# Optimization experiments

Measured on AMD Instinct MI355X. Metric: run time of the kernel, lower is better.

## Reference

```python
import jax, jax.numpy as jnp
import numpy as np

B, N, D, H, C = 4, 512, 128, 128, 3


def setup_inputs() -> dict:
    key = jax.random.key(0)
    k1, k2, k3, k4, k5 = jax.random.split(key, 5)
    s1 = 1.0 / np.sqrt(2 * D)  # torch Linear default init scale (uniform bound); randn is fine for a numerics baseline
    s2 = 1.0 / np.sqrt(H)
    return {
        "h_dense": jax.random.normal(k1, (B, N, D), dtype=jnp.float32),
        "W1": jax.random.normal(k2, (H, 2 * D), dtype=jnp.float32) * s1,
        "b1": jax.random.normal(k3, (H,), dtype=jnp.float32) * s1,
        "W2": jax.random.normal(k4, (C, H), dtype=jnp.float32) * s2,
        "b2": jax.random.normal(k5, (C,), dtype=jnp.float32) * s2,
    }


def reference(h_dense, W1, b1, W2, b2):
    # Linear(concat(h_src, h_dst)) == h_src @ W1[:, :D].T + h_dst @ W1[:, D:].T + b1
    # which avoids materializing the (B, N, N, 2D) concat tensor (same math).
    d = h_dense.shape[-1]
    a = jnp.einsum("bnd,hd->bnh", h_dense, W1[:, :d])  # src projection (B, N, H)
    b = jnp.einsum("bnd,hd->bnh", h_dense, W1[:, d:])  # dst projection (B, N, H)
    pre = a[:, :, None, :] + b[:, None, :, :] + b1      # (B, N, N, H)
    act = jax.nn.silu(pre)
    logits = jnp.einsum("bijh,ch->bijc", act, W2) + b2  # (B, N, N, C)
    # symmetrize over the pair axes (dropout is identity in eval mode)
    return (logits + jnp.swapaxes(logits, 1, 2)) * 0.5
```

## Files before the change

### kernel.cpp

```cpp
#include <hip/hip_runtime.h>
#include <hip/hip_fp16.h>

#define B_ 4
#define N_ 512
#define D_ 128
#define H_ 128
#define C_ 3

#define NEG_LOG2E   (-1.4426950408889634f)
#define NEG_HALF_LN2 (-0.34657359027997264f)

typedef _Float16 half8  __attribute__((ext_vector_type(8)));
typedef _Float16 half4v __attribute__((ext_vector_type(4)));

__device__ __forceinline__ float exp2_fast(float x) {
    return __builtin_amdgcn_exp2f(x);
}

__global__ __launch_bounds__(256) void proj_gemm(
    const float* __restrict__ hd, const float* __restrict__ W1,
    const float* __restrict__ b1, _Float16* __restrict__ At, _Float16* __restrict__ Bt)
{
    __shared__ float hsT[64][36];
    __shared__ float wt [64][68];
    const int m0      = blockIdx.x * 32;
    const int by      = blockIdx.y;
    const int halfSel = by >> 1;
    const int wrow0   = (by & 1) * 64;

    const int t  = threadIdx.x;
    const int r  = t >> 4, c4 = t & 15;
    const int tx = t & 15, ty = t >> 4;

    float acc[2][4] = {};

    for (int kc = 0; kc < 2; ++kc) {
        if (kc) __syncthreads();
        #pragma unroll
        for (int i = 0; i < 2; ++i) {
            const int m = r + 16 * i;
            float4 v = *(const float4*)&hd[(m0 + m) * D_ + kc * 64 + 4 * c4];
            hsT[4 * c4 + 0][m] = v.x; hsT[4 * c4 + 1][m] = v.y;
            hsT[4 * c4 + 2][m] = v.z; hsT[4 * c4 + 3][m] = v.w;
        }
        #pragma unroll
        for (int i = 0; i < 4; ++i) {
            const int o = r + 16 * i;
            float4 v = *(const float4*)&W1[(wrow0 + o) * (2 * D_) + halfSel * D_ + kc * 64 + 4 * c4];
            wt[4 * c4 + 0][o] = v.x; wt[4 * c4 + 1][o] = v.y;
            wt[4 * c4 + 2][o] = v.z; wt[4 * c4 + 3][o] = v.w;
        }
        __syncthreads();
        #pragma unroll 8
        for (int k = 0; k < 64; ++k) {
            float2 a  = *(const float2*)&hsT[k][2 * ty];
            float4 bv = *(const float4*)&wt [k][4 * tx];
            acc[0][0] = fmaf(a.x, bv.x, acc[0][0]); acc[0][1] = fmaf(a.x, bv.y, acc[0][1]);
            acc[0][2] = fmaf(a.x, bv.z, acc[0][2]); acc[0][3] = fmaf(a.x, bv.w, acc[0][3]);
            acc[1][0] = fmaf(a.y, bv.x, acc[1][0]); acc[1][1] = fmaf(a.y, bv.y, acc[1][1]);
            acc[1][2] = fmaf(a.y, bv.z, acc[1][2]); acc[1][3] = fmaf(a.y, bv.w, acc[1][3]);
        }
    }

    _Float16* dst = halfSel ? Bt : At;
    const int ocol = wrow0 + 4 * tx;
    float4 bias = make_float4(0.f, 0.f, 0.f, 0.f);
    if (!halfSel) bias = *(const float4*)&b1[ocol];
    #pragma unroll
    for (int i = 0; i < 2; ++i) {
        half4v o;
        o[0] = (_Float16)((acc[i][0] + bias.x) * NEG_LOG2E);
        o[1] = (_Float16)((acc[i][1] + bias.y) * NEG_LOG2E);
        o[2] = (_Float16)((acc[i][2] + bias.z) * NEG_LOG2E);
        o[3] = (_Float16)((acc[i][3] + bias.w) * NEG_LOG2E);
        *(half4v*)&dst[(m0 + 2 * ty + i) * H_ + ocol] = o;
    }
}

__global__ __launch_bounds__(256, 4) void pair_kernel(
    const _Float16* __restrict__ At, const _Float16* __restrict__ Bt,
    const float* __restrict__ W2, const float* __restrict__ b2,
    float* __restrict__ out)
{
    __shared__ _Float16 tiles[8][16 * 64];
    const int T = N_ / 16;
    int tp = blockIdx.x;
    const int b = blockIdx.y;
    int I = 0;
    while (tp >= T - I) { tp -= T - I; ++I; }
    const int J = I + tp;

    const int tid = threadIdx.x;
    const int stile = tid >> 6;
    const int srow  = (tid >> 2) & 15;
    const int scc   = tid & 3;
    const _Float16* gsrc = ((stile & 2) ? Bt : At)
        + (size_t)(b * N_ + ((stile & 1) ? J : I) * 16 + srow) * H_;
    _Float16* ybase = &tiles[stile][srow * 64];
    _Float16* ebase = &tiles[stile + 4][srow * 64];
    const int sxor = srow & 7;

    const int ti = tid >> 4, tj = tid & 15;
    const int xI = ti & 7, xJ = tj & 7;

    float acc0a = 0.f, acc1a = 0.f, acc2a = 0.f;
    float acc0b = 0.f, acc1b = 0.f, acc2b = 0.f;

    for (int ph = 0; ph < 2; ++ph) {
        if (ph) __syncthreads();
        #pragma unroll
        for (int q = 0; q < 2; ++q) {
            const int c = scc + 4 * q;
            half8 yv = *(const half8*)&gsrc[ph * 64 + c * 8];
            half8 ev;
            #pragma unroll
            for (int e = 0; e < 8; ++e)
                ev[e] = (_Float16)exp2_fast((float)yv[e]);
            const int cs = (c ^ sxor) * 8;
            *(half8*)&ybase[cs] = yv;
            *(half8*)&ebase[cs] = ev;
        }
        __syncthreads();

        #pragma unroll 2
        for (int c = 0; c < 8; ++c) {
            const int oI = ti * 64 + ((c ^ xI) * 8);
            const int oJ = tj * 64 + ((c ^ xJ) * 8);
            half8 yAI = *(const half8*)&tiles[0][oI];
            half8 yAJ = *(const half8*)&tiles[1][oJ];
            half8 yBI = *(const half8*)&tiles[2][oI];
            half8 yBJ = *(const half8*)&tiles[3][oJ];
            half8 eAI = *(const half8*)&tiles[4][oI];
            half8 eAJ = *(const half8*)&tiles[5][oJ];
            half8 eBI = *(const half8*)&tiles[6][oI];
            half8 eBJ = *(const half8*)&tiles[7][oJ];

            half8 y1 = yAI + yBJ;
            half8 y2 = yAJ + yBI;
            half8 e1 = eAI * eBJ;
            half8 e2 = eAJ * eBI;
            half8 d1 = e1 + (_Float16)1.0f;
            half8 d2 = e2 + (_Float16)1.0f;
            half8 pp = d1 * d2;
            half8 num = y1 * d2 + y2 * d1;

            const int hb = ph * 64 + c * 8;
            float4 w0a = *(const float4*)&W2[hb],          w0b = *(const float4*)&W2[hb + 4];
            float4 w1a = *(const float4*)&W2[H_ + hb],     w1b = *(const float4*)&W2[H_ + hb + 4];
            float4 w2a = *(const float4*)&W2[2 * H_ + hb], w2b = *(const float4*)&W2[2 * H_ + hb + 4];
            const float w0[8] = {w0a.x, w0a.y, w0a.z, w0a.w, w0b.x, w0b.y, w0b.z, w0b.w};
            const float w1[8] = {w1a.x, w1a.y, w1a.z, w1a.w, w1b.x, w1b.y, w1b.z, w1b.w};
            const float w2[8] = {w2a.x, w2a.y, w2a.z, w2a.w, w2b.x, w2b.y, w2b.z, w2b.w};

            #pragma unroll
            for (int e = 0; e < 8; e += 2) {
                const float sa = (float)num[e]     * __builtin_amdgcn_rcpf((float)pp[e]);
                const float sb = (float)num[e + 1] * __builtin_amdgcn_rcpf((float)pp[e + 1]);
                acc0a = fmaf(sa, w0[e],     acc0a);
                acc1a = fmaf(sa, w1[e],     acc1a);
                acc2a = fmaf(sa, w2[e],     acc2a);
                acc0b = fmaf(sb, w0[e + 1], acc0b);
                acc1b = fmaf(sb, w1[e + 1], acc1b);
                acc2b = fmaf(sb, w2[e + 1], acc2b);
            }
        }
    }

    const float o0 = fmaf(NEG_HALF_LN2, acc0a + acc0b, b2[0]);
    const float o1 = fmaf(NEG_HALF_LN2, acc1a + acc1b, b2[1]);
    const float o2 = fmaf(NEG_HALF_LN2, acc2a + acc2b, b2[2]);
    const int i = I * 16 + ti, j = J * 16 + tj;
    float* p1 = out + ((size_t)(b * N_ + i) * N_ + j) * C_;
    float* p2 = out + ((size_t)(b * N_ + j) * N_ + i) * C_;
    p1[0] = o0; p1[1] = o1; p1[2] = o2;
    p2[0] = o0; p2[1] = o1; p2[2] = o2;
}

extern "C" void kernel_launch(void* const* d_in, const int* in_sizes, int n_in,
                              void* d_out, int out_size, void* d_ws, size_t ws_size,
                              hipStream_t stream) {
    const float* hd = (const float*)d_in[0];
    const float* W1 = (const float*)d_in[1];
    const float* b1 = (const float*)d_in[2];
    const float* W2 = (const float*)d_in[3];
    const float* b2 = (const float*)d_in[4];
    float* out = (float*)d_out;

    _Float16* At = (_Float16*)d_ws;
    _Float16* Bt = At + B_ * N_ * H_;

    proj_gemm<<<dim3((B_ * N_) / 32, 4), dim3(256), 0, stream>>>(hd, W1, b1, At, Bt);

    const int T = N_ / 16;
    pair_kernel<<<dim3(T * (T + 1) / 2, B_), dim3(256), 0, stream>>>(At, Bt, W2, b2, out);
}
```

Baseline: 39.25 us.

## Enlarge pair tiles to 32x32 with 2x2 register blocking per thread

Each pair_kernel block now covers a 32x32 (i,j) tile, and each thread computes four output pairs. Every LDS-loaded row vector is reused across two pairs, and the W2 loads and exp2 preprocessing are amortized over more outputs. The cost is four times fewer blocks (528 vs 2112 over B=4), occupancy lowered to 2 waves, more registers and 32 KB of LDS per block. Diagonal blocks still do redundant symmetric work.

```diff
diff --git a/kernel.cpp b/kernel.cpp
--- a/kernel.cpp
+++ b/kernel.cpp
@@ -77,13 +77,13 @@
     }
 }
 
-__global__ __launch_bounds__(256, 4) void pair_kernel(
+__global__ __launch_bounds__(256, 2) void pair_kernel(
     const _Float16* __restrict__ At, const _Float16* __restrict__ Bt,
     const float* __restrict__ W2, const float* __restrict__ b2,
     float* __restrict__ out)
 {
-    __shared__ _Float16 tiles[8][16 * 64];
-    const int T = N_ / 16;
+    __shared__ _Float16 tiles[8][32 * 64];
+    const int T = N_ / 32;
     int tp = blockIdx.x;
     const int b = blockIdx.y;
     int I = 0;
@@ -92,10 +92,11 @@
 
     const int tid = threadIdx.x;
     const int stile = tid >> 6;
-    const int srow  = (tid >> 2) & 15;
-    const int scc   = tid & 3;
+    const int lane  = tid & 63;
+    const int srow  = lane >> 1;
+    const int shalf = lane & 1;
     const _Float16* gsrc = ((stile & 2) ? Bt : At)
-        + (size_t)(b * N_ + ((stile & 1) ? J : I) * 16 + srow) * H_;
+        + (size_t)(b * N_ + ((stile & 1) ? J : I) * 32 + srow) * H_;
     _Float16* ybase = &tiles[stile][srow * 64];
     _Float16* ebase = &tiles[stile + 4][srow * 64];
     const int sxor = srow & 7;
@@ -103,14 +104,13 @@
     const int ti = tid >> 4, tj = tid & 15;
     const int xI = ti & 7, xJ = tj & 7;
 
-    float acc0a = 0.f, acc1a = 0.f, acc2a = 0.f;
-    float acc0b = 0.f, acc1b = 0.f, acc2b = 0.f;
+    float acc[4][3] = {};
 
     for (int ph = 0; ph < 2; ++ph) {
         if (ph) __syncthreads();
         #pragma unroll
-        for (int q = 0; q < 2; ++q) {
-            const int c = scc + 4 * q;
+        for (int q = 0; q < 4; ++q) {
+            const int c = shalf * 4 + q;
             half8 yv = *(const half8*)&gsrc[ph * 64 + c * 8];
             half8 ev;
             #pragma unroll
@@ -122,27 +122,19 @@
         }
         __syncthreads();
 
-        #pragma unroll 2
         for (int c = 0; c < 8; ++c) {
-            const int oI = ti * 64 + ((c ^ xI) * 8);
-            const int oJ = tj * 64 + ((c ^ xJ) * 8);
-            half8 yAI = *(const half8*)&tiles[0][oI];
-            half8 yAJ = *(const half8*)&tiles[1][oJ];
-            half8 yBI = *(const half8*)&tiles[2][oI];
-            half8 yBJ = *(const half8*)&tiles[3][oJ];
-            half8 eAI = *(const half8*)&tiles[4][oI];
-            half8 eAJ = *(const half8*)&tiles[5][oJ];
-            half8 eBI = *(const half8*)&tiles[6][oI];
-            half8 eBJ = *(const half8*)&tiles[7][oJ];
-
-            half8 y1 = yAI + yBJ;
-            half8 y2 = yAJ + yBI;
-            half8 e1 = eAI * eBJ;
-            half8 e2 = eAJ * eBI;
-            half8 d1 = e1 + (_Float16)1.0f;
-            half8 d2 = e2 + (_Float16)1.0f;
-            half8 pp = d1 * d2;
-            half8 num = y1 * d2 + y2 * d1;
+            const int oI0 =  ti       * 64 + ((c ^ xI) * 8);
+            const int oI1 = (ti + 16) * 64 + ((c ^ xI) * 8);
+            const int oJ0 =  tj       * 64 + ((c ^ xJ) * 8);
+            const int oJ1 = (tj + 16) * 64 + ((c ^ xJ) * 8);
+            half8 yAI0 = *(const half8*)&tiles[0][oI0], yAI1 = *(const half8*)&tiles[0][oI1];
+            half8 yAJ0 = *(const half8*)&tiles[1][oJ0], yAJ1 = *(const half8*)&tiles[1][oJ1];
+            half8 yBI0 = *(const half8*)&tiles[2][oI0], yBI1 = *(const half8*)&tiles[2][oI1];
+            half8 yBJ0 = *(const half8*)&tiles[3][oJ0], yBJ1 = *(const half8*)&tiles[3][oJ1];
+            half8 eAI0 = *(const half8*)&tiles[4][oI0], eAI1 = *(const half8*)&tiles[4][oI1];
+            half8 eAJ0 = *(const half8*)&tiles[5][oJ0], eAJ1 = *(const half8*)&tiles[5][oJ1];
+            half8 eBI0 = *(const half8*)&tiles[6][oI0], eBI1 = *(const half8*)&tiles[6][oI1];
+            half8 eBJ0 = *(const half8*)&tiles[7][oJ0], eBJ1 = *(const half8*)&tiles[7][oJ1];
 
             const int hb = ph * 64 + c * 8;
             float4 w0a = *(const float4*)&W2[hb],          w0b = *(const float4*)&W2[hb + 4];
@@ -152,28 +144,46 @@
             const float w1[8] = {w1a.x, w1a.y, w1a.z, w1a.w, w1b.x, w1b.y, w1b.z, w1b.w};
             const float w2[8] = {w2a.x, w2a.y, w2a.z, w2a.w, w2b.x, w2b.y, w2b.z, w2b.w};
 
-            #pragma unroll
-            for (int e = 0; e < 8; e += 2) {
-                const float sa = (float)num[e]     * __builtin_amdgcn_rcpf((float)pp[e]);
-                const float sb = (float)num[e + 1] * __builtin_amdgcn_rcpf((float)pp[e + 1]);
-                acc0a = fmaf(sa, w0[e],     acc0a);
-                acc1a = fmaf(sa, w1[e],     acc1a);
-                acc2a = fmaf(sa, w2[e],     acc2a);
-                acc0b = fmaf(sb, w0[e + 1], acc0b);
-                acc1b = fmaf(sb, w1[e + 1], acc1b);
-                acc2b = fmaf(sb, w2[e + 1], acc2b);
+            #define SILU4(p, yAIv, yBIv, eAIv, eBIv, yAJv, yBJv, eAJv, eBJv)      \
+            {                                                                     \
+                half8 y1 = (yAIv) + (yBJv);                                       \
+                half8 y2 = (yAJv) + (yBIv);                                       \
+                half8 e1 = (eAIv) * (eBJv);                                       \
+                half8 e2 = (eAJv) * (eBIv);                                       \
+                half8 d1 = e1 + (_Float16)1.0f;                                   \
+                half8 d2 = e2 + (_Float16)1.0f;                                   \
+                half8 pp = d1 * d2;                                               \
+                half8 num = y1 * d2 + y2 * d1;                                    \
+                _Pragma("unroll")                                                 \
+                for (int e = 0; e < 8; ++e) {                                     \
+                    const float s = (float)num[e]                                 \
+                                  * __builtin_amdgcn_rcpf((float)pp[e]);          \
+                    acc[p][0] = fmaf(s, w0[e], acc[p][0]);                        \
+                    acc[p][1] = fmaf(s, w1[e], acc[p][1]);                        \
+                    acc[p][2] = fmaf(s, w2[e], acc[p][2]);                        \
+                }                                                                 \
             }
-        }
-    }
-
-    const float o0 = fmaf(NEG_HALF_LN2, acc0a + acc0b, b2[0]);
-    const float o1 = fmaf(NEG_HALF_LN2, acc1a + acc1b, b2[1]);
-    const float o2 = fmaf(NEG_HALF_LN2, acc2a + acc2b, b2[2]);
-    const int i = I * 16 + ti, j = J * 16 + tj;
-    float* p1 = out + ((size_t)(b * N_ + i) * N_ + j) * C_;
-    float* p2 = out + ((size_t)(b * N_ + j) * N_ + i) * C_;
-    p1[0] = o0; p1[1] = o1; p1[2] = o2;
-    p2[0] = o0; p2[1] = o1; p2[2] = o2;
+            SILU4(0, yAI0, yBI0, eAI0, eBI0, yAJ0, yBJ0, eAJ0, eBJ0)
+            SILU4(1, yAI0, yBI0, eAI0, eBI0, yAJ1, yBJ1, eAJ1, eBJ1)
+            SILU4(2, yAI1, yBI1, eAI1, eBI1, yAJ0, yBJ0, eAJ0, eBJ0)
+            SILU4(3, yAI1, yBI1, eAI1, eBI1, yAJ1, yBJ1, eAJ1, eBJ1)
+            #undef SILU4
+        }
+    }
+
+    const float b20 = b2[0], b21 = b2[1], b22 = b2[2];
+    #pragma unroll
+    for (int p = 0; p < 4; ++p) {
+        const int i = I * 32 + ti + (p >> 1) * 16;
+        const int j = J * 32 + tj + (p & 1) * 16;
+        const float o0 = fmaf(NEG_HALF_LN2, acc[p][0], b20);
+        const float o1 = fmaf(NEG_HALF_LN2, acc[p][1], b21);
+        const float o2 = fmaf(NEG_HALF_LN2, acc[p][2], b22);
+        float* p1 = out + ((size_t)(b * N_ + i) * N_ + j) * C_;
+        float* p2 = out + ((size_t)(b * N_ + j) * N_ + i) * C_;
+        p1[0] = o0; p1[1] = o1; p1[2] = o2;
+        p2[0] = o0; p2[1] = o1; p2[2] = o2;
+    }
 }
 
 extern "C" void kernel_launch(void* const* d_in, const int* in_sizes, int n_in,
@@ -191,6 +201,6 @@
 
     proj_gemm<<<dim3((B_ * N_) / 32, 4), dim3(256), 0, stream>>>(hd, W1, b1, At, Bt);
 
-    const int T = N_ / 16;
+    const int T = N_ / 32;
     pair_kernel<<<dim3(T * (T + 1) / 2, B_), dim3(256), 0, stream>>>(At, Bt, W2, b2, out);
 }
```

Result: slower. 48.71 us (+24.1%).
